# Optimization experiments

Measured on AMD Instinct MI355X. Metric: run time of the kernel, lower is better.

The kernel has to match this reference:

```python
import jax, jax.numpy as jnp
import numpy as np

B, N, D, H, V, L = 32, 64, 128, 256, 32000, 3  # batch, nodes, embd_dim, msg_hid, vocab, num_layers


def _linear_init(key, fan_in, fan_out):
    k1, k2 = jax.random.split(key)
    s = 1.0 / np.sqrt(fan_in)
    W = jax.random.uniform(k1, (fan_out, fan_in), jnp.float32, -s, s)
    b = jax.random.uniform(k2, (fan_out,), jnp.float32, -s, s)
    return W, b


def setup_inputs() -> dict:
    key = jax.random.key(0)
    ks = jax.random.split(key, 7)
    x = jax.random.randint(ks[0], (B, N), 0, V)                      # token ids
    arcs = jax.random.randint(ks[1], (B, N, N), 0, 2).astype(jnp.int32)
    lengths = jnp.ones((B, N), dtype=jnp.int32)                      # unused by forward
    embd_table = jax.random.normal(ks[2], (V, D), jnp.float32)
    embd_table = embd_table.at[0].set(0.0)                           # padding_idx = 0
    W1_0, b1_0 = _linear_init(ks[3], 2 * D, H)
    W2_0, b2_0 = _linear_init(ks[4], H, D)
    W1_1, b1_1 = _linear_init(ks[5], 2 * D, H)
    W2_1, b2_1 = _linear_init(ks[6], H, D)
    return dict(x=x, arcs=arcs, lengths=lengths, embd_table=embd_table,
                W1_0=W1_0, b1_0=b1_0, W2_0=W2_0, b2_0=b2_0,
                W1_1=W1_1, b1_1=b1_1, W2_1=W2_1, b2_1=b2_1)


def reference(x, arcs, lengths, embd_table,
              W1_0, b1_0, W2_0, b2_0, W1_1, b1_1, W2_1, b2_1):
    # Edge k = (row=k//n, col=k%n). Caller passes senders_idxs=one_hot(cols),
    # receivers_idxs=one_hot(rows); aggregation sums messages over rows.
    # Equivalent gather/scatter expressed as (B,n,n,·) broadcast + sum over axis 2.
    b, n = x.shape
    d = embd_table.shape[1]
    E = embd_table[x]                                   # (B,n,d)
    a = arcs.astype(E.dtype)[..., None]                 # (B,n,n,1) edge-type-1 weight

    def mlp(pre, W1, b1, W2, b2):
        h = jax.nn.relu(jnp.einsum('brce,he->brch', pre, W1) + b1)
        return jax.nn.relu(jnp.einsum('brch,dh->brcd', h, W2) + b2)

    for _ in range(L):
        senders = jnp.broadcast_to(E[:, None, :, :], (b, n, n, d))    # col embedding
        receivers = jnp.broadcast_to(E[:, :, None, :], (b, n, n, d))  # row embedding
        pre = jnp.concatenate([senders, receivers], axis=-1)          # (B,n,n,2d)
        m0 = mlp(pre, W1_0, b1_0, W2_0, b2_0)
        m1 = mlp(pre, W1_1, b1_1, W2_1, b2_1)
        all_msgs = m0 * (1.0 - a) + m1 * a                            # (B,n,n,d)
        agg = all_msgs.sum(axis=2)                                    # scatter-add over rows
        E = E + agg
    return E[:, 0, :]
```

## Files before the change

### kernel.cpp

```cpp
#include <hip/hip_runtime.h>
#include <hip/hip_bf16.h>
#include <stdint.h>


#define NB 32
#define NN 64
#define DD 128
#define HH 256

typedef __attribute__((ext_vector_type(4))) float f32x4;
typedef __attribute__((ext_vector_type(8))) _Float16 f16x8;

__device__ __forceinline__ uint64_t cvt4h(f32x4 v) {
  union { _Float16 h[4]; uint64_t u; } x;
  x.h[0] = (_Float16)v[0]; x.h[1] = (_Float16)v[1];
  x.h[2] = (_Float16)v[2]; x.h[3] = (_Float16)v[3];
  return x.u;
}

__global__ __launch_bounds__(256) void k_setup(const int* __restrict__ x,
                                               const float* __restrict__ table,
                                               float* __restrict__ E0,
                                               const float* __restrict__ W1_0,
                                               const float* __restrict__ W1_1,
                                               const float* __restrict__ W2_0,
                                               const float* __restrict__ W2_1,
                                               _Float16* __restrict__ W1fp,
                                               _Float16* __restrict__ W2fp) {
  int bid = blockIdx.x, t = threadIdx.x;
  if (bid < 256) {
    int i = bid * 256 + t;
    int node = i >> 5;
    ((f32x4*)E0)[i] = ((const f32x4*)table)[(size_t)x[node] * 32 + (i & 31)];
  } else {
    int tid = (bid - 256) * 256 + t;
    const float* src; uint64_t* dst; int off;
    if (tid < 32768) {
      src = (tid < 16384) ? W1_0 : W1_1;
      off = tid & 16383;
      dst = (uint64_t*)W1fp + (tid >> 14) * 16384 + off;
    } else {
      int t2 = tid - 32768;
      src = (t2 < 8192) ? W2_0 : W2_1;
      off = t2 & 8191;
      dst = (uint64_t*)W2fp + (t2 >> 13) * 8192 + off;
    }
    *dst = cvt4h(((const f32x4*)src)[off]);
  }
}

template <int NSP, int NR>
__global__ __launch_bounds__(256) void k_fused(
    const float* __restrict__ E0,
    const float* __restrict__ spA,
    const float* __restrict__ spB,
    float* __restrict__ spOut,
    const _Float16* __restrict__ W1fp,
    const _Float16* __restrict__ W2fp,
    const float* __restrict__ b1_0, const float* __restrict__ b1_1,
    const float* __restrict__ b2_0, const float* __restrict__ b2_1,
    const int* __restrict__ arcs) {
  __shared__ char lds[53248];
  char* Els = lds;
  char* Tsl = lds + 16384;
  char* Trl = lds + 49152;

  int t = threadIdx.x;
  int rg = blockIdx.x, b = blockIdx.y, p = blockIdx.z;
  int rbase = rg * 8;
  int lane = t & 63, w = t >> 6, col = lane & 15, khi = lane >> 4;
  const f32x4 z4 = {0.f, 0.f, 0.f, 0.f};

  {
    const f32x4* e0 = (const f32x4*)(E0 + (size_t)b * NN * DD);
    const f32x4* a0 = (const f32x4*)(spA + (size_t)b * NN * DD);
    const f32x4* a1 = (const f32x4*)(spA + (size_t)(NB + b) * NN * DD);
    const f32x4* c0 = (const f32x4*)(spB + (size_t)b * NN * DD);
    const f32x4* c1 = (const f32x4*)(spB + (size_t)(NB + b) * NN * DD);
#pragma unroll
    for (int ii = 0; ii < 8; ++ii) {
      int idx = ii * 256 + t;
      f32x4 v = e0[idx];
      if (NSP >= 1) v += a0[idx] + a1[idx];
      if (NSP >= 2) v += c0[idx] + c1[idx];
      int node = idx >> 5, ck = idx & 31;
      *(uint64_t*)(Els + node * 256 + ((ck * 8) ^ ((node & 7) << 4))) = cvt4h(v);
    }
  }
  __syncthreads();

  const _Float16* Wq = W1fp + p * 65536;
  const float* b1p = p ? b1_1 : b1_0;
  int eswz = (col & 7) << 4;

#pragma unroll
  for (int nth = 0; nth < 2; ++nth) {
    f16x8 bfr[2][4];
#pragma unroll
    for (int nt = 0; nt < 2; ++nt) {
      int h = w * 64 + nth * 32 + nt * 16 + col;
#pragma unroll
      for (int ks = 0; ks < 4; ++ks)
        bfr[nt][ks] = *(const f16x8*)(Wq + h * 256 + ks * 32 + khi * 8);
    }
    f32x4 tacc[4][2];
#pragma unroll
    for (int mt = 0; mt < 4; ++mt) { tacc[mt][0] = z4; tacc[mt][1] = z4; }
#pragma unroll
    for (int ks = 0; ks < 4; ++ks) {
      f16x8 a[4];
#pragma unroll
      for (int mt = 0; mt < 4; ++mt)
        a[mt] = *(const f16x8*)(Els + (mt * 16 + col) * 256 +
                                ((ks * 64 + khi * 16) ^ eswz));
#pragma unroll
      for (int mt = 0; mt < 4; ++mt) {
        tacc[mt][0] = __builtin_amdgcn_mfma_f32_16x16x32_f16(a[mt], bfr[0][ks],
                                                             tacc[mt][0], 0, 0, 0);
        tacc[mt][1] = __builtin_amdgcn_mfma_f32_16x16x32_f16(a[mt], bfr[1][ks],
                                                             tacc[mt][1], 0, 0, 0);
      }
    }
#pragma unroll
    for (int mt = 0; mt < 4; ++mt)
#pragma unroll
      for (int nt = 0; nt < 2; ++nt) {
        int h = w * 64 + nth * 32 + nt * 16 + col;
#pragma unroll
        for (int j = 0; j < 4; ++j) {
          int c = mt * 16 + khi * 4 + j;
          *(_Float16*)(Tsl + c * 512 + ((h * 2) ^ ((c & 7) << 4))) =
              (_Float16)tacc[mt][nt][j];
        }
      }
  }
  {
    int mt_t = (NR == 1) ? 0 : (rg >> 1);
    int sel = (NR == 1) ? 0 : (rg & 1);
#pragma unroll
    for (int nth = 0; nth < 2; ++nth) {
      f16x8 bfr[2][4];
#pragma unroll
      for (int nt = 0; nt < 2; ++nt) {
        int h = w * 64 + nth * 32 + nt * 16 + col;
#pragma unroll
        for (int ks = 0; ks < 4; ++ks)
          bfr[nt][ks] = *(const f16x8*)(Wq + h * 256 + 128 + ks * 32 + khi * 8);
      }
      f32x4 tacc[2] = {z4, z4};
#pragma unroll
      for (int ks = 0; ks < 4; ++ks) {
        f16x8 a = *(const f16x8*)(Els + (mt_t * 16 + col) * 256 +
                                  ((ks * 64 + khi * 16) ^ eswz));
        tacc[0] = __builtin_amdgcn_mfma_f32_16x16x32_f16(a, bfr[0][ks], tacc[0], 0, 0, 0);
        tacc[1] = __builtin_amdgcn_mfma_f32_16x16x32_f16(a, bfr[1][ks], tacc[1], 0, 0, 0);
      }
      if ((khi >> 1) == sel) {
#pragma unroll
        for (int nt = 0; nt < 2; ++nt) {
          int h = w * 64 + nth * 32 + nt * 16 + col;
          float bb = b1p[h];
#pragma unroll
          for (int j = 0; j < 4; ++j) {
            int lr = (khi & 1) * 4 + j;
            *(_Float16*)(Trl + lr * 512 + ((h * 2) ^ ((lr & 7) << 4))) =
                (_Float16)(tacc[nt][j] + bb);
          }
        }
      }
    }
  }
  __syncthreads();

  int d0 = w * 32 + col;
  const _Float16* W2p = W2fp + p * 32768;
  f16x8 bv[2][8];
#pragma unroll
  for (int nt = 0; nt < 2; ++nt)
#pragma unroll
    for (int ks = 0; ks < 8; ++ks)
      bv[nt][ks] = *(const f16x8*)(W2p + (d0 + nt * 16) * 256 + ks * 32 + khi * 8);
  const float* b2p = p ? b2_1 : b2_0;
  float b2v[2] = {b2p[d0], b2p[d0 + 16]};
  const char* tsb = Tsl + col * 512;

#pragma unroll 1
  for (int r = 0; r < NR; ++r) {
    asm volatile("" : "+v"(bv[0][0]), "+v"(bv[0][1]), "+v"(bv[0][2]), "+v"(bv[0][3]),
                      "+v"(bv[0][4]), "+v"(bv[0][5]), "+v"(bv[0][6]), "+v"(bv[0][7]),
                      "+v"(bv[1][0]), "+v"(bv[1][1]), "+v"(bv[1][2]), "+v"(bv[1][3]),
                      "+v"(bv[1][4]), "+v"(bv[1][5]), "+v"(bv[1][6]), "+v"(bv[1][7]));
    f32x4 acc[4][2];
#pragma unroll
    for (int mt = 0; mt < 4; ++mt) { acc[mt][0] = z4; acc[mt][1] = z4; }
#pragma unroll
    for (int ks = 0; ks < 8; ++ks) {
      f16x8 trv = *(const f16x8*)(Trl + r * 512 +
                                  ((ks * 64 + khi * 16) ^ ((r & 7) << 4)));
#pragma unroll
      for (int mt = 0; mt < 4; ++mt) {
        f16x8 ts = *(const f16x8*)(tsb + mt * 8192 + ((ks * 64 + khi * 16) ^ eswz));
        f16x8 zv = {};
        f16x8 a = __builtin_elementwise_max(ts + trv, zv);
        acc[mt][0] = __builtin_amdgcn_mfma_f32_16x16x32_f16(a, bv[0][ks],
                                                            acc[mt][0], 0, 0, 0);
        acc[mt][1] = __builtin_amdgcn_mfma_f32_16x16x32_f16(a, bv[1][ks],
                                                            acc[mt][1], 0, 0, 0);
      }
    }
    int rr = rbase + r;
    const int* arow = arcs + ((size_t)(b * NN + rr)) * NN;
    float s0 = 0.f, s1 = 0.f;
#pragma unroll
    for (int mt = 0; mt < 4; ++mt) {
      const int4 av = *(const int4*)(arow + mt * 16 + khi * 4);
#pragma unroll
      for (int j = 0; j < 4; ++j) {
        int ai = (j == 0) ? av.x : (j == 1) ? av.y : (j == 2) ? av.z : av.w;
        float wgt = p ? (float)ai : 1.0f - (float)ai;
        s0 = fmaf(wgt, fmaxf(acc[mt][0][j] + b2v[0], 0.f), s0);
        s1 = fmaf(wgt, fmaxf(acc[mt][1][j] + b2v[1], 0.f), s1);
      }
    }
    s0 += __shfl_xor(s0, 16); s0 += __shfl_xor(s0, 32);
    s1 += __shfl_xor(s1, 16); s1 += __shfl_xor(s1, 32);
    if (khi == 0) {
      if (NR == 1) {
        float* o = spOut + (size_t)(p * NB + b) * DD;
        o[d0] = s0; o[d0 + 16] = s1;
      } else {
        float* o = spOut + ((size_t)(p * NB + b) * NN + rr) * DD;
        o[d0] = s0; o[d0 + 16] = s1;
      }
    }
  }
}

__global__ __launch_bounds__(256) void k_out(const float* __restrict__ E0,
                                             const float* __restrict__ spA,
                                             const float* __restrict__ spB,
                                             const float* __restrict__ spC,
                                             float* __restrict__ out) {
  int i = blockIdx.x * 256 + threadIdx.x;
  int b = i >> 7, d = i & 127;
  float acc = E0[(size_t)b * NN * DD + d];
  acc += spA[(size_t)b * NN * DD + d] + spA[(size_t)(NB + b) * NN * DD + d];
  acc += spB[(size_t)b * NN * DD + d] + spB[(size_t)(NB + b) * NN * DD + d];
  acc += spC[(size_t)b * DD + d] + spC[(size_t)(NB + b) * DD + d];
  out[i] = acc;
}

extern "C" void kernel_launch(void* const* d_in, const int* in_sizes, int n_in,
                              void* d_out, int out_size, void* d_ws, size_t ws_size,
                              hipStream_t stream) {
  const int* x       = (const int*)d_in[0];
  const int* arcs    = (const int*)d_in[1];
  const float* table = (const float*)d_in[3];
  const float* W1_0  = (const float*)d_in[4];
  const float* b1_0  = (const float*)d_in[5];
  const float* W2_0  = (const float*)d_in[6];
  const float* b2_0  = (const float*)d_in[7];
  const float* W1_1  = (const float*)d_in[8];
  const float* b1_1  = (const float*)d_in[9];
  const float* W2_1  = (const float*)d_in[10];
  const float* b2_1  = (const float*)d_in[11];
  float* out = (float*)d_out;

  char* ws = (char*)d_ws;
  float* E0        = (float*)ws;
  _Float16* W1fp   = (_Float16*)(ws + (1u << 20));
  _Float16* W2fp   = (_Float16*)(ws + (1u << 20) + (256u << 10));
  float* SpA       = (float*)(ws + (2u << 20));
  float* SpB       = (float*)(ws + (4u << 20));
  float* SpC       = (float*)(ws + (6u << 20));

  k_setup<<<448, 256, 0, stream>>>(x, table, E0, W1_0, W1_1, W2_0, W2_1,
                                   W1fp, W2fp);
  k_fused<0, 8><<<dim3(8, 32, 2), 256, 0, stream>>>(
      E0, E0, E0, SpA, W1fp, W2fp, b1_0, b1_1, b2_0, b2_1, arcs);
  k_fused<1, 8><<<dim3(8, 32, 2), 256, 0, stream>>>(
      E0, SpA, E0, SpB, W1fp, W2fp, b1_0, b1_1, b2_0, b2_1, arcs);
  k_fused<2, 1><<<dim3(1, 32, 2), 256, 0, stream>>>(
      E0, SpA, SpB, SpC, W1fp, W2fp, b1_0, b1_1, b2_0, b2_1, arcs);
  k_out<<<16, 256, 0, stream>>>(E0, SpA, SpB, SpC, out);
}
```

Baseline: 102.1 us.

## Split embedding sum into separate fp16 kernel and read E from global

Moves the per-layer embedding accumulation (E0 plus the partial message sums) and the fp16 conversion out of every fused block into a standalone k_esum kernel. Each k_fused block then loads fp16 embeddings straight from global memory instead of staging them in LDS. This removes the summation that 16 blocks per batch were repeating, and cuts LDS use so more blocks can be resident. The message loop also drops its asm register pinning and switches to unroll 2. The cost is three extra kernel launches and global-latency loads inside the first GEMM stages.

```diff
diff --git a/kernel.cpp b/kernel.cpp
--- a/kernel.cpp
+++ b/kernel.cpp
@@ -49,49 +49,46 @@
   }
 }
 
-template <int NSP, int NR>
+template <int NSP>
+__global__ __launch_bounds__(256) void k_esum(const float* __restrict__ E0,
+                                              const float* __restrict__ spA,
+                                              const float* __restrict__ spB,
+                                              _Float16* __restrict__ E16) {
+  int i = blockIdx.x * 256 + threadIdx.x;
+  f32x4 v = ((const f32x4*)E0)[i];
+  if (NSP >= 1) {
+#pragma unroll
+    for (int s = 0; s < 2; ++s) v += ((const f32x4*)spA)[s * 65536 + i];
+  }
+  if (NSP >= 2) {
+#pragma unroll
+    for (int s = 0; s < 2; ++s) v += ((const f32x4*)spB)[s * 65536 + i];
+  }
+  ((uint64_t*)E16)[i] = cvt4h(v);
+}
+
+template <int NR>
 __global__ __launch_bounds__(256) void k_fused(
-    const float* __restrict__ E0,
-    const float* __restrict__ spA,
-    const float* __restrict__ spB,
+    const _Float16* __restrict__ E16,
     float* __restrict__ spOut,
     const _Float16* __restrict__ W1fp,
     const _Float16* __restrict__ W2fp,
     const float* __restrict__ b1_0, const float* __restrict__ b1_1,
     const float* __restrict__ b2_0, const float* __restrict__ b2_1,
     const int* __restrict__ arcs) {
-  __shared__ char lds[53248];
-  char* Els = lds;
-  char* Tsl = lds + 16384;
-  char* Trl = lds + 49152;
+  __shared__ char lds[36864];
+  char* Tsl = lds;
+  char* Trl = lds + 32768;
 
   int t = threadIdx.x;
   int rg = blockIdx.x, b = blockIdx.y, p = blockIdx.z;
-  int rbase = rg * 8;
+  int rbase = rg * NR;
   int lane = t & 63, w = t >> 6, col = lane & 15, khi = lane >> 4;
   const f32x4 z4 = {0.f, 0.f, 0.f, 0.f};
-
-  {
-    const f32x4* e0 = (const f32x4*)(E0 + (size_t)b * NN * DD);
-    const f32x4* a0 = (const f32x4*)(spA + (size_t)b * NN * DD);
-    const f32x4* a1 = (const f32x4*)(spA + (size_t)(NB + b) * NN * DD);
-    const f32x4* c0 = (const f32x4*)(spB + (size_t)b * NN * DD);
-    const f32x4* c1 = (const f32x4*)(spB + (size_t)(NB + b) * NN * DD);
-#pragma unroll
-    for (int ii = 0; ii < 8; ++ii) {
-      int idx = ii * 256 + t;
-      f32x4 v = e0[idx];
-      if (NSP >= 1) v += a0[idx] + a1[idx];
-      if (NSP >= 2) v += c0[idx] + c1[idx];
-      int node = idx >> 5, ck = idx & 31;
-      *(uint64_t*)(Els + node * 256 + ((ck * 8) ^ ((node & 7) << 4))) = cvt4h(v);
-    }
-  }
-  __syncthreads();
+  const _Float16* Eb = E16 + (size_t)b * NN * DD;
 
   const _Float16* Wq = W1fp + p * 65536;
   const float* b1p = p ? b1_1 : b1_0;
-  int eswz = (col & 7) << 4;
 
 #pragma unroll
   for (int nth = 0; nth < 2; ++nth) {
@@ -110,9 +107,10 @@
     for (int ks = 0; ks < 4; ++ks) {
       f16x8 a[4];
 #pragma unroll
-      for (int mt = 0; mt < 4; ++mt)
-        a[mt] = *(const f16x8*)(Els + (mt * 16 + col) * 256 +
-                                ((ks * 64 + khi * 16) ^ eswz));
+      for (int mt = 0; mt < 4; ++mt) {
+        int node = mt * 16 + col;
+        a[mt] = *(const f16x8*)(Eb + node * DD + ks * 32 + khi * 8);
+      }
 #pragma unroll
       for (int mt = 0; mt < 4; ++mt) {
         tacc[mt][0] = __builtin_amdgcn_mfma_f32_16x16x32_f16(a[mt], bfr[0][ks],
@@ -150,8 +148,8 @@
       f32x4 tacc[2] = {z4, z4};
 #pragma unroll
       for (int ks = 0; ks < 4; ++ks) {
-        f16x8 a = *(const f16x8*)(Els + (mt_t * 16 + col) * 256 +
-                                  ((ks * 64 + khi * 16) ^ eswz));
+        int node = mt_t * 16 + col;
+        f16x8 a = *(const f16x8*)(Eb + node * DD + ks * 32 + khi * 8);
         tacc[0] = __builtin_amdgcn_mfma_f32_16x16x32_f16(a, bfr[0][ks], tacc[0], 0, 0, 0);
         tacc[1] = __builtin_amdgcn_mfma_f32_16x16x32_f16(a, bfr[1][ks], tacc[1], 0, 0, 0);
       }
@@ -182,14 +180,9 @@
       bv[nt][ks] = *(const f16x8*)(W2p + (d0 + nt * 16) * 256 + ks * 32 + khi * 8);
   const float* b2p = p ? b2_1 : b2_0;
   float b2v[2] = {b2p[d0], b2p[d0 + 16]};
-  const char* tsb = Tsl + col * 512;
-
-#pragma unroll 1
+
+#pragma unroll 2
   for (int r = 0; r < NR; ++r) {
-    asm volatile("" : "+v"(bv[0][0]), "+v"(bv[0][1]), "+v"(bv[0][2]), "+v"(bv[0][3]),
-                      "+v"(bv[0][4]), "+v"(bv[0][5]), "+v"(bv[0][6]), "+v"(bv[0][7]),
-                      "+v"(bv[1][0]), "+v"(bv[1][1]), "+v"(bv[1][2]), "+v"(bv[1][3]),
-                      "+v"(bv[1][4]), "+v"(bv[1][5]), "+v"(bv[1][6]), "+v"(bv[1][7]));
     f32x4 acc[4][2];
 #pragma unroll
     for (int mt = 0; mt < 4; ++mt) { acc[mt][0] = z4; acc[mt][1] = z4; }
@@ -199,7 +192,9 @@
                                   ((ks * 64 + khi * 16) ^ ((r & 7) << 4)));
 #pragma unroll
       for (int mt = 0; mt < 4; ++mt) {
-        f16x8 ts = *(const f16x8*)(tsb + mt * 8192 + ((ks * 64 + khi * 16) ^ eswz));
+        int c = mt * 16 + col;
+        f16x8 ts = *(const f16x8*)(Tsl + c * 512 +
+                                   ((ks * 64 + khi * 16) ^ ((c & 7) << 4)));
         f16x8 zv = {};
         f16x8 a = __builtin_elementwise_max(ts + trv, zv);
         acc[mt][0] = __builtin_amdgcn_mfma_f32_16x16x32_f16(a, bv[0][ks],
@@ -270,17 +265,21 @@
   float* E0        = (float*)ws;
   _Float16* W1fp   = (_Float16*)(ws + (1u << 20));
   _Float16* W2fp   = (_Float16*)(ws + (1u << 20) + (256u << 10));
+  _Float16* E16    = (_Float16*)(ws + (1u << 20) + (384u << 10));
   float* SpA       = (float*)(ws + (2u << 20));
   float* SpB       = (float*)(ws + (4u << 20));
   float* SpC       = (float*)(ws + (6u << 20));
 
   k_setup<<<448, 256, 0, stream>>>(x, table, E0, W1_0, W1_1, W2_0, W2_1,
                                    W1fp, W2fp);
-  k_fused<0, 8><<<dim3(8, 32, 2), 256, 0, stream>>>(
-      E0, E0, E0, SpA, W1fp, W2fp, b1_0, b1_1, b2_0, b2_1, arcs);
-  k_fused<1, 8><<<dim3(8, 32, 2), 256, 0, stream>>>(
-      E0, SpA, E0, SpB, W1fp, W2fp, b1_0, b1_1, b2_0, b2_1, arcs);
-  k_fused<2, 1><<<dim3(1, 32, 2), 256, 0, stream>>>(
-      E0, SpA, SpB, SpC, W1fp, W2fp, b1_0, b1_1, b2_0, b2_1, arcs);
+  k_esum<0><<<256, 256, 0, stream>>>(E0, E0, E0, E16);
+  k_fused<8><<<dim3(8, 32, 2), 256, 0, stream>>>(
+      E16, SpA, W1fp, W2fp, b1_0, b1_1, b2_0, b2_1, arcs);
+  k_esum<1><<<256, 256, 0, stream>>>(E0, SpA, E0, E16);
+  k_fused<8><<<dim3(8, 32, 2), 256, 0, stream>>>(
+      E16, SpB, W1fp, W2fp, b1_0, b1_1, b2_0, b2_1, arcs);
+  k_esum<2><<<256, 256, 0, stream>>>(E0, SpA, SpB, E16);
+  k_fused<1><<<dim3(1, 32, 2), 256, 0, stream>>>(
+      E16, SpC, W1fp, W2fp, b1_0, b1_1, b2_0, b2_1, arcs);
   k_out<<<16, 256, 0, stream>>>(E0, SpA, SpB, SpC, out);
 }
```

Result: slower. 114.7 us (+12.2%).
